# Kernel tuning notes

Hardware: AMD Instinct MI355X
Metric: run time of the kernel (lower is better)

Reference implementation:

```python
import jax, jax.numpy as jnp
import numpy as np

U, I, D, B, T = 100000, 50000, 64, 8192, 30
EUI, EII, L = 1600000, 800000, 2
LN_EPS = 1e-5
BEH_SCALE = 0.35
REG_COEF = 1e-4


def _ln(x, g, b):
    mu = jnp.mean(x, axis=-1, keepdims=True)
    var = jnp.mean((x - mu) ** 2, axis=-1, keepdims=True)
    return (x - mu) * jax.lax.rsqrt(var + LN_EPS) * g + b


def setup_inputs() -> dict:
    key = jax.random.key(0)
    ks = jax.random.split(key, 32)
    s = 0.1
    n = lambda k, shp: jax.random.normal(k, shp, dtype=jnp.float32) * s
    return {
        "user_emb": n(ks[0], (U, D)),
        "item_emb": n(ks[1], (I, D)),
        "beh_emb": n(ks[2], (4, D)),
        "t_w1": n(ks[3], (1, D)),
        "t_b1": jnp.zeros((D,), jnp.float32),
        "t_w2": n(ks[4], (D, D)),
        "t_b2": jnp.zeros((D,), jnp.float32),
        "gru_w_ih": n(ks[5], (D, 3 * D)),
        "gru_w_hh": n(ks[6], (D, 3 * D)),
        "gru_b_ih": jnp.zeros((3 * D,), jnp.float32),
        "gru_b_hh": jnp.zeros((3 * D,), jnp.float32),
        "gnn_user_w": n(ks[7], (L, D, D)),
        "gnn_user_b": jnp.zeros((L, D), jnp.float32),
        "gnn_item_w": n(ks[8], (L, D, D)),
        "gnn_item_b": jnp.zeros((L, D), jnp.float32),
        "ln_g": jnp.ones((D,), jnp.float32),
        "ln_b": jnp.zeros((D,), jnp.float32),
        "ui_vals": jax.random.uniform(ks[9], (EUI,), dtype=jnp.float32) * 0.1,
        "adj_vals": jax.random.uniform(ks[10], (EII,), dtype=jnp.float32) * 0.1,
        "seq_delta_days": jax.random.uniform(ks[11], (B, T), dtype=jnp.float32) * 100.0,
        "ui_rows": jax.random.randint(ks[12], (EUI,), 0, U),
        "ui_cols": jax.random.randint(ks[13], (EUI,), 0, I),
        "adj_rows": jax.random.randint(ks[14], (EII,), 0, I),
        "adj_cols": jax.random.randint(ks[15], (EII,), 0, I),
        "seq_items": jax.random.randint(ks[16], (B, T), 0, I),
        "seq_behaviors": jax.random.randint(ks[17], (B, T), 0, 4),
        "seq_len": jax.random.randint(ks[18], (B,), 1, T + 1),
        "user_idx": jax.random.randint(ks[19], (B,), 0, U),
        "pos_item_idx": jax.random.randint(ks[20], (B,), 0, I),
        "neg_item_idx": jax.random.randint(ks[21], (B,), 0, I),
        "pos_behavior": jax.random.randint(ks[22], (B,), 0, 4),
    }


def _forward(user_emb, item_emb, beh_emb, t_w1, t_b1, t_w2, t_b2,
             gru_w_ih, gru_w_hh, gru_b_ih, gru_b_hh,
             gnn_user_w, gnn_user_b, gnn_item_w, gnn_item_b,
             ln_g, ln_b, ui_vals, adj_vals, seq_delta_days,
             ui_rows, ui_cols, adj_rows, adj_cols,
             seq_items, seq_behaviors, seq_len,
             user_idx, pos_item_idx, neg_item_idx, pos_behavior):
    seg = jax.ops.segment_sum
    u, it = user_emb, item_emb
    # spatial propagation (sparse mm via edge-list segment sums); dropout off (eval)
    for l in range(L):
        agg_u = seg(ui_vals[:, None] * it[ui_cols], ui_rows, num_segments=U)       # ui_norm @ i
        agg_i_t = seg(adj_vals[:, None] * it[adj_cols], adj_rows, num_segments=I)  # item_adj @ i
        agg_i_u = seg(ui_vals[:, None] * u[ui_rows], ui_cols, num_segments=I)      # ui_norm.T @ u
        u = jax.nn.relu((u + agg_u) @ gnn_user_w[l] + gnn_user_b[l])
        it = jax.nn.relu((it + agg_i_t + agg_i_u) @ gnn_item_w[l] + gnn_item_b[l])
    # sequence encoding
    seq_x = it[seq_items] + BEH_SCALE * beh_emb[seq_behaviors]                     # [B,T,D]
    t_in = jnp.log1p(seq_delta_days)[..., None]                                    # [B,T,1]
    seq_x = seq_x + jax.nn.relu(t_in @ t_w1 + t_b1) @ t_w2 + t_b2
    seq_x = _ln(seq_x, ln_g, ln_b)
    mask = jnp.arange(T)[:, None] < seq_len[None, :]                               # [T,B]
    xs = jnp.transpose(seq_x, (1, 0, 2))                                           # [T,B,D]
    h0 = jnp.zeros((B, D), seq_x.dtype)

    def step(h, inputs):
        x_t, m_t = inputs
        gi = x_t @ gru_w_ih + gru_b_ih
        gh = h @ gru_w_hh + gru_b_hh
        i_r, i_z, i_n = jnp.split(gi, 3, axis=-1)
        h_r, h_z, h_n = jnp.split(gh, 3, axis=-1)
        r = jax.nn.sigmoid(i_r + h_r)
        z = jax.nn.sigmoid(i_z + h_z)
        nn_ = jnp.tanh(i_n + r * h_n)
        h_new = (1.0 - z) * nn_ + z * h
        return jnp.where(m_t[:, None], h_new, h), None

    seq_repr, _ = jax.lax.scan(step, h0, (xs, mask))                               # hidden at last valid step
    # BPR scoring
    u_final = _ln(u[user_idx] + seq_repr, ln_g, ln_b)
    pos = it[pos_item_idx]
    neg = it[neg_item_idx]
    pos_s = jnp.sum(u_final * pos, axis=-1)
    neg_s = jnp.sum(u_final * neg, axis=-1)
    w_map = jnp.array([1.0, 1.25, 1.6, 2.1], dtype=pos_s.dtype)
    bw = w_map[jnp.clip(pos_behavior, 0, 3)]
    bpr = jnp.mean(-jax.nn.log_sigmoid(pos_s - neg_s) * bw)
    reg = (jnp.mean(jnp.linalg.norm(u_final, axis=-1))
           + jnp.mean(jnp.linalg.norm(pos, axis=-1))
           + jnp.mean(jnp.linalg.norm(neg, axis=-1))) * REG_COEF
    return bpr + reg


def reference(user_emb, item_emb, beh_emb, t_w1, t_b1, t_w2, t_b2,
              gru_w_ih, gru_w_hh, gru_b_ih, gru_b_hh,
              gnn_user_w, gnn_user_b, gnn_item_w, gnn_item_b,
              ln_g, ln_b, ui_vals, adj_vals, seq_delta_days,
              ui_rows, ui_cols, adj_rows, adj_cols,
              seq_items, seq_behaviors, seq_len,
              user_idx, pos_item_idx, neg_item_idx, pos_behavior):
    return _forward(user_emb, item_emb, beh_emb, t_w1, t_b1, t_w2, t_b2,
                    gru_w_ih, gru_w_hh, gru_b_ih, gru_b_hh,
                    gnn_user_w, gnn_user_b, gnn_item_w, gnn_item_b,
                    ln_g, ln_b, ui_vals, adj_vals, seq_delta_days,
                    ui_rows, ui_cols, adj_rows, adj_cols,
                    seq_items, seq_behaviors, seq_len,
                    user_idx, pos_item_idx, neg_item_idx, pos_behavior)
```

## Files before the change

### kernel.cpp

```cpp
#include <hip/hip_runtime.h>
#include <math.h>

#define U_N 100000
#define I_N 50000
#define DD  64
#define BB  8192
#define TT  30
#define N_EUI 1600000
#define N_EII 800000
#define LN_EPS_ 1e-5f
#define BEH_SCALE_ 0.35f
#define REG_COEF_ 1e-4f

typedef unsigned short us_t;

__device__ __forceinline__ float wave_sum64(float v) {
#pragma unroll
  for (int o = 32; o > 0; o >>= 1) v += __shfl_xor(v, o, 64);
  return v;
}

__device__ __forceinline__ float rdlane(float v, int k) {
  return __int_as_float(__builtin_amdgcn_readlane(__float_as_int(v), k));
}

__device__ __forceinline__ us_t f2bf(float f) {
  unsigned u = __float_as_uint(f);
  u += 0x7fffu + ((u >> 16) & 1u);
  return (us_t)(u >> 16);
}
__device__ __forceinline__ float bf2f(us_t h) {
  return __uint_as_float((unsigned)h << 16);
}

__device__ __forceinline__ void fma4(float* acc, float s, float4 w4) {
  acc[0] = fmaf(s, w4.x, acc[0]);
  acc[1] = fmaf(s, w4.y, acc[1]);
  acc[2] = fmaf(s, w4.z, acc[2]);
  acc[3] = fmaf(s, w4.w, acc[3]);
}

__global__ __launch_bounds__(256) void to_bf16(const float* __restrict__ in,
                                               us_t* __restrict__ out,
                                               long n4) {
  for (long i = (long)blockIdx.x * blockDim.x + threadIdx.x; i < n4;
       i += (long)gridDim.x * blockDim.x) {
    float4 f = ((const float4*)in)[i];
    ushort4 o;
    o.x = f2bf(f.x); o.y = f2bf(f.y); o.z = f2bf(f.z); o.w = f2bf(f.w);
    ((ushort4*)out)[i] = o;
  }
}


__global__ __launch_bounds__(256) void hist_kernel(
    const int* __restrict__ rows, int nE, int* __restrict__ cnt) {
  for (long e = (long)blockIdx.x * blockDim.x + threadIdx.x; e < nE;
       e += (long)gridDim.x * blockDim.x)
    atomicAdd(&cnt[rows[e]], 1);
}

__global__ __launch_bounds__(1024) void ex_scan(
    const int* __restrict__ cnt, int n, int* __restrict__ offs,
    int* __restrict__ cursor) {
  __shared__ int part[1024];
  const int tid = threadIdx.x;
  const int chunk = (n + 1023) / 1024;
  const int lo = tid * chunk;
  const int hi = min(lo + chunk, n);
  int s = 0;
  for (int i = lo; i < hi; ++i) s += cnt[i];
  part[tid] = s;
  __syncthreads();
  for (int off = 1; off < 1024; off <<= 1) {
    int v = part[tid];
    int add = (tid >= off) ? part[tid - off] : 0;
    __syncthreads();
    part[tid] = v + add;
    __syncthreads();
  }
  int base = (tid == 0) ? 0 : part[tid - 1];
  for (int i = lo; i < hi; ++i) {
    int c = cnt[i];
    offs[i] = base;
    cursor[i] = base;
    base += c;
  }
  if (tid == 0) offs[n] = part[1023];
}

__global__ __launch_bounds__(256) void csr_fill(
    const int* __restrict__ drows, const int* __restrict__ srows,
    const float* __restrict__ vals, int nE, int* __restrict__ cursor,
    int2* __restrict__ pairs) {
  for (long e = (long)blockIdx.x * blockDim.x + threadIdx.x; e < nE;
       e += (long)gridDim.x * blockDim.x) {
    int d = drows[e];
    int pos = atomicAdd(&cursor[d], 1);
    pairs[pos] = make_int2(srows[e], __float_as_int(vals[e]));
  }
}


__global__ __launch_bounds__(256) void gnn_user_layer(
    const float* __restrict__ cur_u, const us_t* __restrict__ src_bf,
    const int* __restrict__ offs, const int2* __restrict__ pairs,
    const float* __restrict__ W, const float* __restrict__ bias,
    float* __restrict__ out, us_t* __restrict__ out_bf) {
  __shared__ float Wl[DD * DD];
  for (int i = threadIdx.x; i < DD * DD; i += blockDim.x) Wl[i] = W[i];
  __syncthreads();
  const int lane = threadIdx.x & 63;
  const float bn = bias[lane];
  long wid = ((long)blockIdx.x * blockDim.x + threadIdx.x) >> 6;
  long nw = ((long)gridDim.x * blockDim.x) >> 6;
  for (long r = wid; r < U_N; r += nw) {
    float acc = cur_u[r * DD + lane], acc2 = 0.f;
    int j = offs[r], j1 = offs[r + 1];
    for (; j + 1 < j1; j += 2) {
      int2 p0 = pairs[j], p1 = pairs[j + 1];
      acc = fmaf(__int_as_float(p0.y), bf2f(src_bf[(long)p0.x * DD + lane]), acc);
      acc2 = fmaf(__int_as_float(p1.y), bf2f(src_bf[(long)p1.x * DD + lane]), acc2);
    }
    if (j < j1) {
      int2 p = pairs[j];
      acc = fmaf(__int_as_float(p.y), bf2f(src_bf[(long)p.x * DD + lane]), acc);
    }
    acc += acc2;
    float y = bn;
#pragma unroll
    for (int k = 0; k < DD; ++k)
      y = fmaf(rdlane(acc, k), Wl[k * DD + lane], y);
    y = fmaxf(y, 0.f);
    out[r * DD + lane] = y;
    if (out_bf) out_bf[r * DD + lane] = f2bf(y);
  }
}

__global__ __launch_bounds__(256) void gnn_item_layer(
    const float* __restrict__ cur_it, const us_t* __restrict__ it_bf,
    const us_t* __restrict__ u_bf, const int* __restrict__ offsA,
    const int2* __restrict__ pairsA, const int* __restrict__ offsB,
    const int2* __restrict__ pairsB, const float* __restrict__ W,
    const float* __restrict__ bias, float* __restrict__ out,
    us_t* __restrict__ out_bf) {
  __shared__ float Wl[DD * DD];
  for (int i = threadIdx.x; i < DD * DD; i += blockDim.x) Wl[i] = W[i];
  __syncthreads();
  const int lane = threadIdx.x & 63;
  const float bn = bias[lane];
  long wid = ((long)blockIdx.x * blockDim.x + threadIdx.x) >> 6;
  long nw = ((long)gridDim.x * blockDim.x) >> 6;
  for (long r = wid; r < I_N; r += nw) {
    float acc = cur_it[r * DD + lane], acc2 = 0.f;
    int j = offsA[r], j1 = offsA[r + 1];
    for (; j + 1 < j1; j += 2) {
      int2 p0 = pairsA[j], p1 = pairsA[j + 1];
      acc = fmaf(__int_as_float(p0.y), bf2f(it_bf[(long)p0.x * DD + lane]), acc);
      acc2 = fmaf(__int_as_float(p1.y), bf2f(it_bf[(long)p1.x * DD + lane]), acc2);
    }
    if (j < j1) {
      int2 p = pairsA[j];
      acc = fmaf(__int_as_float(p.y), bf2f(it_bf[(long)p.x * DD + lane]), acc);
    }
    j = offsB[r];
    j1 = offsB[r + 1];
    for (; j + 1 < j1; j += 2) {
      int2 p0 = pairsB[j], p1 = pairsB[j + 1];
      acc = fmaf(__int_as_float(p0.y), bf2f(u_bf[(long)p0.x * DD + lane]), acc);
      acc2 = fmaf(__int_as_float(p1.y), bf2f(u_bf[(long)p1.x * DD + lane]), acc2);
    }
    if (j < j1) {
      int2 p = pairsB[j];
      acc = fmaf(__int_as_float(p.y), bf2f(u_bf[(long)p.x * DD + lane]), acc);
    }
    acc += acc2;
    float y = bn;
#pragma unroll
    for (int k = 0; k < DD; ++k)
      y = fmaf(rdlane(acc, k), Wl[k * DD + lane], y);
    y = fmaxf(y, 0.f);
    out[r * DD + lane] = y;
    if (out_bf) out_bf[r * DD + lane] = f2bf(y);
  }
}

__global__ __launch_bounds__(256) void gnn_user_sel(
    const float* __restrict__ u_a, const us_t* __restrict__ ita_bf,
    const int* __restrict__ user_idx, const int* __restrict__ offs,
    const int2* __restrict__ pairs, const float* __restrict__ W,
    const float* __restrict__ bias, float* __restrict__ out) {
  __shared__ float Wl[DD * DD];
  for (int i = threadIdx.x; i < DD * DD; i += blockDim.x) Wl[i] = W[i];
  __syncthreads();
  const int lane = threadIdx.x & 63;
  const float bn = bias[lane];
  long wid = ((long)blockIdx.x * blockDim.x + threadIdx.x) >> 6;
  long nw = ((long)gridDim.x * blockDim.x) >> 6;
  for (long b = wid; b < BB; b += nw) {
    int r = user_idx[b];
    float acc = u_a[(long)r * DD + lane], acc2 = 0.f;
    int j = offs[r], j1 = offs[r + 1];
    for (; j + 1 < j1; j += 2) {
      int2 p0 = pairs[j], p1 = pairs[j + 1];
      acc = fmaf(__int_as_float(p0.y), bf2f(ita_bf[(long)p0.x * DD + lane]), acc);
      acc2 = fmaf(__int_as_float(p1.y), bf2f(ita_bf[(long)p1.x * DD + lane]), acc2);
    }
    if (j < j1) {
      int2 p = pairs[j];
      acc = fmaf(__int_as_float(p.y), bf2f(ita_bf[(long)p.x * DD + lane]), acc);
    }
    acc += acc2;
    float y = bn;
#pragma unroll
    for (int k = 0; k < DD; ++k)
      y = fmaf(rdlane(acc, k), Wl[k * DD + lane], y);
    out[b * DD + lane] = fmaxf(y, 0.f);
  }
}


__global__ __launch_bounds__(256) void seq_encode_gi4(
    const float* __restrict__ itf, const float* __restrict__ beh_emb,
    const float* __restrict__ t_w1, const float* __restrict__ t_b1,
    const float* __restrict__ t_w2, const float* __restrict__ t_b2,
    const float* __restrict__ ln_g, const float* __restrict__ ln_b,
    const float* __restrict__ Wih, const float* __restrict__ bih,
    const float* __restrict__ delta, const int* __restrict__ items,
    const int* __restrict__ behs, us_t* __restrict__ gi) {
  __shared__ float W2q[DD * DD];
  __shared__ float WIq[192 * DD];
  for (int i = threadIdx.x; i < DD * DD; i += 256) {
    int k = i >> 6, c = i & 63;
    W2q[(k >> 2) * 256 + c * 4 + (k & 3)] = t_w2[i];
  }
  for (int i = threadIdx.x; i < DD * 192; i += 256) {
    int k = i / 192, c = i - k * 192;
    WIq[(k >> 2) * 768 + c * 4 + (k & 3)] = Wih[i];
  }
  __syncthreads();
  const int lane = threadIdx.x & 63;
  const float w1 = t_w1[lane], b1 = t_b1[lane], b2 = t_b2[lane];
  const float g = ln_g[lane], bo = ln_b[lane];
  const float bi0 = bih[lane], bi1 = bih[64 + lane], bi2 = bih[128 + lane];
  long wid = ((long)blockIdx.x * blockDim.x + threadIdx.x) >> 6;
  long nw = ((long)gridDim.x * blockDim.x) >> 6;
  const long NR = (long)BB * TT;
  for (long r4 = wid * 4; r4 < NR; r4 += nw * 4) {
    float xv[4], tmp[4];
#pragma unroll
    for (int i = 0; i < 4; ++i) {
      long r = r4 + i;
      int it = items[r];
      int bh = behs[r];
      xv[i] = itf[(long)it * DD + lane] + BEH_SCALE_ * beh_emb[bh * DD + lane];
      float tv = log1pf(delta[r]);
      tmp[i] = fmaxf(fmaf(tv, w1, b1), 0.f);
    }
    float y[4] = {b2, b2, b2, b2};
#pragma unroll 4
    for (int k4 = 0; k4 < 16; ++k4) {
      float4 w4 = *(const float4*)&W2q[k4 * 256 + lane * 4];
#pragma unroll
      for (int i = 0; i < 4; ++i) {
        y[i] = fmaf(rdlane(tmp[i], 4 * k4 + 0), w4.x, y[i]);
        y[i] = fmaf(rdlane(tmp[i], 4 * k4 + 1), w4.y, y[i]);
        y[i] = fmaf(rdlane(tmp[i], 4 * k4 + 2), w4.z, y[i]);
        y[i] = fmaf(rdlane(tmp[i], 4 * k4 + 3), w4.w, y[i]);
      }
    }
    float xo[4];
#pragma unroll
    for (int i = 0; i < 4; ++i) {
      float x = xv[i] + y[i];
      float mu = wave_sum64(x) * (1.f / DD);
      float xc = x - mu;
      float var = wave_sum64(xc * xc) * (1.f / DD);
      xo[i] = xc * rsqrtf(var + LN_EPS_) * g + bo;
    }
    float gA[4] = {bi0, bi0, bi0, bi0};
    float gB[4] = {bi1, bi1, bi1, bi1};
    float gC[4] = {bi2, bi2, bi2, bi2};
#pragma unroll 4
    for (int k4 = 0; k4 < 16; ++k4) {
      float4 wA = *(const float4*)&WIq[k4 * 768 + lane * 4];
      float4 wB = *(const float4*)&WIq[k4 * 768 + (64 + lane) * 4];
      float4 wC = *(const float4*)&WIq[k4 * 768 + (128 + lane) * 4];
#pragma unroll
      for (int i = 0; i < 4; ++i) {
        float s0 = rdlane(xo[i], 4 * k4 + 0);
        float s1 = rdlane(xo[i], 4 * k4 + 1);
        float s2 = rdlane(xo[i], 4 * k4 + 2);
        float s3 = rdlane(xo[i], 4 * k4 + 3);
        gA[i] = fmaf(s0, wA.x, gA[i]); gA[i] = fmaf(s1, wA.y, gA[i]);
        gA[i] = fmaf(s2, wA.z, gA[i]); gA[i] = fmaf(s3, wA.w, gA[i]);
        gB[i] = fmaf(s0, wB.x, gB[i]); gB[i] = fmaf(s1, wB.y, gB[i]);
        gB[i] = fmaf(s2, wB.z, gB[i]); gB[i] = fmaf(s3, wB.w, gB[i]);
        gC[i] = fmaf(s0, wC.x, gC[i]); gC[i] = fmaf(s1, wC.y, gC[i]);
        gC[i] = fmaf(s2, wC.z, gC[i]); gC[i] = fmaf(s3, wC.w, gC[i]);
      }
    }
#pragma unroll
    for (int i = 0; i < 4; ++i) {
      us_t* go = gi + (r4 + i) * 192;
      go[lane] = f2bf(gA[i]);
      go[64 + lane] = f2bf(gB[i]);
      go[128 + lane] = f2bf(gC[i]);
    }
  }
}

#define GHSTR 34

__global__ __launch_bounds__(256, 4) void gru_scan4(
    const us_t* __restrict__ gi, const float* __restrict__ Whh,
    const float* __restrict__ bhh, const int* __restrict__ seq_len,
    float* __restrict__ hfin) {
  __shared__ float sW[DD * 192];
  __shared__ float hT[DD * GHSTR];
  const int tid = threadIdx.x;
  for (int i = tid; i < DD * 192; i += 256) sW[i] = Whh[i];
  const int ct = tid & 15, rt = tid >> 4;
  const int d0 = ct * 4, r0 = rt * 2;
  const int row0 = blockIdx.x * 32;
  float bR[4], bZ[4], bN[4];
#pragma unroll
  for (int dd = 0; dd < 4; ++dd) {
    bR[dd] = bhh[d0 + dd];
    bZ[dd] = bhh[64 + d0 + dd];
    bN[dd] = bhh[128 + d0 + dd];
  }
  const int sl0 = seq_len[row0 + r0], sl1 = seq_len[row0 + r0 + 1];
  float h0[4] = {0.f, 0.f, 0.f, 0.f}, h1[4] = {0.f, 0.f, 0.f, 0.f};
  const us_t* ga = gi + (long)(row0 + r0) * TT * 192;
  const us_t* gb = gi + (long)(row0 + r0 + 1) * TT * 192;
  ushort4 pa0 = *(const ushort4*)(ga + d0);
  ushort4 pa1 = *(const ushort4*)(ga + 64 + d0);
  ushort4 pa2 = *(const ushort4*)(ga + 128 + d0);
  ushort4 pb0 = *(const ushort4*)(gb + d0);
  ushort4 pb1 = *(const ushort4*)(gb + 64 + d0);
  ushort4 pb2 = *(const ushort4*)(gb + 128 + d0);
  __syncthreads();

  for (int t = 0; t < TT; ++t) {
#pragma unroll
    for (int dd = 0; dd < 4; ++dd) {
      hT[(d0 + dd) * GHSTR + r0] = h0[dd];
      hT[(d0 + dd) * GHSTR + r0 + 1] = h1[dd];
    }
    ushort4 na0, na1, na2, nb0, nb1, nb2;
    if (t + 1 < TT) {
      const us_t* a = ga + (long)(t + 1) * 192;
      const us_t* b = gb + (long)(t + 1) * 192;
      na0 = *(const ushort4*)(a + d0);
      na1 = *(const ushort4*)(a + 64 + d0);
      na2 = *(const ushort4*)(a + 128 + d0);
      nb0 = *(const ushort4*)(b + d0);
      nb1 = *(const ushort4*)(b + 64 + d0);
      nb2 = *(const ushort4*)(b + 128 + d0);
    }
    float aR0[4], aZ0[4], aN0[4], aH0[4];
    float aR1[4], aZ1[4], aN1[4], aH1[4];
    aR0[0] = bR[0] + bf2f(pa0.x); aR0[1] = bR[1] + bf2f(pa0.y);
    aR0[2] = bR[2] + bf2f(pa0.z); aR0[3] = bR[3] + bf2f(pa0.w);
    aZ0[0] = bZ[0] + bf2f(pa1.x); aZ0[1] = bZ[1] + bf2f(pa1.y);
    aZ0[2] = bZ[2] + bf2f(pa1.z); aZ0[3] = bZ[3] + bf2f(pa1.w);
    aN0[0] = bf2f(pa2.x); aN0[1] = bf2f(pa2.y);
    aN0[2] = bf2f(pa2.z); aN0[3] = bf2f(pa2.w);
    aR1[0] = bR[0] + bf2f(pb0.x); aR1[1] = bR[1] + bf2f(pb0.y);
    aR1[2] = bR[2] + bf2f(pb0.z); aR1[3] = bR[3] + bf2f(pb0.w);
    aZ1[0] = bZ[0] + bf2f(pb1.x); aZ1[1] = bZ[1] + bf2f(pb1.y);
    aZ1[2] = bZ[2] + bf2f(pb1.z); aZ1[3] = bZ[3] + bf2f(pb1.w);
    aN1[0] = bf2f(pb2.x); aN1[1] = bf2f(pb2.y);
    aN1[2] = bf2f(pb2.z); aN1[3] = bf2f(pb2.w);
#pragma unroll
    for (int dd = 0; dd < 4; ++dd) {
      aH0[dd] = bN[dd];
      aH1[dd] = bN[dd];
    }
    __syncthreads();
#pragma unroll 8
    for (int k = 0; k < DD; ++k) {
      float2 hh = *(const float2*)&hT[k * GHSTR + r0];
      float4 wr4 = *(const float4*)&sW[k * 192 + d0];
      float4 wz4 = *(const float4*)&sW[k * 192 + 64 + d0];
      float4 wn4 = *(const float4*)&sW[k * 192 + 128 + d0];
      fma4(aR0, hh.x, wr4);
      fma4(aR1, hh.y, wr4);
      fma4(aZ0, hh.x, wz4);
      fma4(aZ1, hh.y, wz4);
      fma4(aH0, hh.x, wn4);
      fma4(aH1, hh.y, wn4);
    }
    const bool m0 = t < sl0, m1 = t < sl1;
#pragma unroll
    for (int dd = 0; dd < 4; ++dd) {
      float rg = 1.f / (1.f + __expf(-aR0[dd]));
      float zg = 1.f / (1.f + __expf(-aZ0[dd]));
      float ng = tanhf(fmaf(rg, aH0[dd], aN0[dd]));
      float hn = fmaf(zg, h0[dd] - ng, ng);
      h0[dd] = m0 ? hn : h0[dd];
      rg = 1.f / (1.f + __expf(-aR1[dd]));
      zg = 1.f / (1.f + __expf(-aZ1[dd]));
      ng = tanhf(fmaf(rg, aH1[dd], aN1[dd]));
      hn = fmaf(zg, h1[dd] - ng, ng);
      h1[dd] = m1 ? hn : h1[dd];
    }
    pa0 = na0; pa1 = na1; pa2 = na2;
    pb0 = nb0; pb1 = nb1; pb2 = nb2;
    __syncthreads();
  }
#pragma unroll
  for (int dd = 0; dd < 4; ++dd) {
    hfin[(long)(row0 + r0) * DD + d0 + dd] = h0[dd];
    hfin[(long)(row0 + r0 + 1) * DD + d0 + dd] = h1[dd];
  }
}


__global__ __launch_bounds__(256) void final_score(
    const float* __restrict__ u_sel, const float* __restrict__ itf,
    const float* __restrict__ hfin, const float* __restrict__ ln_g,
    const float* __restrict__ ln_b, const int* __restrict__ pos_idx,
    const int* __restrict__ neg_idx, const int* __restrict__ pos_beh,
    float* __restrict__ out) {
  __shared__ float partial[4];
  const int lane = threadIdx.x & 63;
  const int wv = threadIdx.x >> 6;
  const float g = ln_g[lane], bo = ln_b[lane];
  float local = 0.f;
  int wid = blockIdx.x * 4 + wv;
  int nw = gridDim.x * 4;
  for (int r = wid; r < BB; r += nw) {
    float uf = u_sel[(long)r * DD + lane] + hfin[(long)r * DD + lane];
    float mu = wave_sum64(uf) * (1.f / DD);
    float xc = uf - mu;
    float var = wave_sum64(xc * xc) * (1.f / DD);
    float un = xc * rsqrtf(var + LN_EPS_) * g + bo;
    float pv = itf[(long)pos_idx[r] * DD + lane];
    float nv = itf[(long)neg_idx[r] * DD + lane];
    float ps = wave_sum64(un * pv);
    float ns = wave_sum64(un * nv);
    float n1 = wave_sum64(un * un);
    float n2 = wave_sum64(pv * pv);
    float n3 = wave_sum64(nv * nv);
    float d = ps - ns;
    float sp = fmaxf(-d, 0.f) + log1pf(__expf(-fabsf(d)));
    int pb = pos_beh[r];
    pb = pb < 0 ? 0 : (pb > 3 ? 3 : pb);
    float bw = pb == 0 ? 1.0f : (pb == 1 ? 1.25f : (pb == 2 ? 1.6f : 2.1f));
    local += sp * bw + REG_COEF_ * (sqrtf(n1) + sqrtf(n2) + sqrtf(n3));
  }
  if (lane == 0) partial[wv] = local;
  __syncthreads();
  if (threadIdx.x == 0) {
    float s = partial[0] + partial[1] + partial[2] + partial[3];
    atomicAdd(out, s * (1.f / BB));
  }
}

extern "C" void kernel_launch(void* const* d_in, const int* in_sizes, int n_in,
                              void* d_out, int out_size, void* d_ws,
                              size_t ws_size, hipStream_t stream) {
  const float* user_emb = (const float*)d_in[0];
  const float* item_emb = (const float*)d_in[1];
  const float* beh_emb = (const float*)d_in[2];
  const float* t_w1 = (const float*)d_in[3];
  const float* t_b1 = (const float*)d_in[4];
  const float* t_w2 = (const float*)d_in[5];
  const float* t_b2 = (const float*)d_in[6];
  const float* gru_w_ih = (const float*)d_in[7];
  const float* gru_w_hh = (const float*)d_in[8];
  const float* gru_b_ih = (const float*)d_in[9];
  const float* gru_b_hh = (const float*)d_in[10];
  const float* gnn_user_w = (const float*)d_in[11];
  const float* gnn_user_b = (const float*)d_in[12];
  const float* gnn_item_w = (const float*)d_in[13];
  const float* gnn_item_b = (const float*)d_in[14];
  const float* ln_g = (const float*)d_in[15];
  const float* ln_b = (const float*)d_in[16];
  const float* ui_vals = (const float*)d_in[17];
  const float* adj_vals = (const float*)d_in[18];
  const float* seq_delta = (const float*)d_in[19];
  const int* ui_rows = (const int*)d_in[20];
  const int* ui_cols = (const int*)d_in[21];
  const int* adj_rows = (const int*)d_in[22];
  const int* adj_cols = (const int*)d_in[23];
  const int* seq_items = (const int*)d_in[24];
  const int* seq_behaviors = (const int*)d_in[25];
  const int* seq_len = (const int*)d_in[26];
  const int* user_idx = (const int*)d_in[27];
  const int* pos_item_idx = (const int*)d_in[28];
  const int* neg_item_idx = (const int*)d_in[29];
  const int* pos_behavior = (const int*)d_in[30];

  float* ws = (float*)d_ws;
  float* u_a = ws;
  float* it_a = u_a + (long)U_N * DD;
  float* it_b = it_a + (long)I_N * DD;
  float* hfin = it_b + (long)I_N * DD;
  float* u_sel = hfin + (long)BB * DD;
  float* end_f = u_sel + (long)BB * DD;

  int2* pairs_ui_row = (int2*)end_f;
  int2* pairs_ui_col = pairs_ui_row + N_EUI;
  int2* pairs_adj = pairs_ui_col + N_EUI;

  us_t* gi = (us_t*)(pairs_adj + N_EII);
  us_t* user_bf = gi + (long)BB * TT * 192;
  us_t* item_bf = user_bf + (long)U_N * DD;
  us_t* ua_bf = item_bf + (long)I_N * DD;
  us_t* ita_bf = ua_bf + (long)U_N * DD;

  int* offs_ui_row = (int*)(ita_bf + (long)I_N * DD);
  int* offs_ui_col = offs_ui_row + (U_N + 1);
  int* offs_adj = offs_ui_col + (I_N + 1);
  int* cur_ui_row = offs_adj + (I_N + 1);
  int* cur_ui_col = cur_ui_row + U_N;
  int* cur_adj = cur_ui_col + I_N;

  hipMemsetAsync(d_out, 0, (size_t)out_size * sizeof(float), stream);
  hipMemsetAsync(cur_ui_row, 0, (size_t)(U_N + I_N + I_N) * sizeof(int),
                 stream);

  to_bf16<<<1024, 256, 0, stream>>>(user_emb, user_bf, (long)U_N * DD / 4);
  to_bf16<<<1024, 256, 0, stream>>>(item_emb, item_bf, (long)I_N * DD / 4);

  hist_kernel<<<2048, 256, 0, stream>>>(ui_rows, N_EUI, cur_ui_row);
  hist_kernel<<<2048, 256, 0, stream>>>(ui_cols, N_EUI, cur_ui_col);
  hist_kernel<<<1024, 256, 0, stream>>>(adj_rows, N_EII, cur_adj);
  ex_scan<<<1, 1024, 0, stream>>>(cur_ui_row, U_N, offs_ui_row, cur_ui_row);
  ex_scan<<<1, 1024, 0, stream>>>(cur_ui_col, I_N, offs_ui_col, cur_ui_col);
  ex_scan<<<1, 1024, 0, stream>>>(cur_adj, I_N, offs_adj, cur_adj);
  csr_fill<<<2048, 256, 0, stream>>>(ui_rows, ui_cols, ui_vals, N_EUI,
                                     cur_ui_row, pairs_ui_row);
  csr_fill<<<2048, 256, 0, stream>>>(ui_cols, ui_rows, ui_vals, N_EUI,
                                     cur_ui_col, pairs_ui_col);
  csr_fill<<<1024, 256, 0, stream>>>(adj_rows, adj_cols, adj_vals, N_EII,
                                     cur_adj, pairs_adj);

  gnn_user_layer<<<2048, 256, 0, stream>>>(user_emb, item_bf, offs_ui_row,
                                           pairs_ui_row, gnn_user_w,
                                           gnn_user_b, u_a, ua_bf);
  gnn_item_layer<<<2048, 256, 0, stream>>>(item_emb, item_bf, user_bf,
                                           offs_adj, pairs_adj, offs_ui_col,
                                           pairs_ui_col, gnn_item_w,
                                           gnn_item_b, it_a, ita_bf);
  gnn_item_layer<<<2048, 256, 0, stream>>>(it_a, ita_bf, ua_bf, offs_adj,
                                           pairs_adj, offs_ui_col,
                                           pairs_ui_col, gnn_item_w + DD * DD,
                                           gnn_item_b + DD, it_b, nullptr);
  gnn_user_sel<<<512, 256, 0, stream>>>(u_a, ita_bf, user_idx, offs_ui_row,
                                        pairs_ui_row, gnn_user_w + DD * DD,
                                        gnn_user_b + DD, u_sel);

  seq_encode_gi4<<<512, 256, 0, stream>>>(it_b, beh_emb, t_w1, t_b1, t_w2,
                                          t_b2, ln_g, ln_b, gru_w_ih,
                                          gru_b_ih, seq_delta, seq_items,
                                          seq_behaviors, gi);

  gru_scan4<<<BB / 32, 256, 0, stream>>>(gi, gru_w_hh, gru_b_hh, seq_len,
                                         hfin);

  final_score<<<256, 256, 0, stream>>>(u_sel, it_b, hfin, ln_g, ln_b,
                                       pos_item_idx, neg_item_idx,
                                       pos_behavior, (float*)d_out);
}
```

Measured before the change: 2.167 ms.

## Use bf16 MFMA for sequence encoder matmuls and merge CSR build kernels

Rewrites the sequence encoder so the time-MLP projection and the GRU input projection run as 16x16x32 bf16 MFMA tiles over 16-row groups. Activations are staged through a swizzled LDS buffer and weights are preconverted to bf16 fragments. Separately, the three histogram, scan and fill launches for CSR construction are each merged into one launch to cut launch overhead. This adds bf16 rounding on the inputs to the time-MLP matmul and more block-level syncs per tile, and the grid is fixed at 480 blocks to cover all rows exactly.

```diff
diff --git a/kernel.cpp b/kernel.cpp
--- a/kernel.cpp
+++ b/kernel.cpp
@@ -13,6 +13,8 @@
 #define REG_COEF_ 1e-4f
 
 typedef unsigned short us_t;
+typedef __attribute__((ext_vector_type(8))) short bf16x8;
+typedef __attribute__((ext_vector_type(4))) float f32x4;
 
 __device__ __forceinline__ float wave_sum64(float v) {
 #pragma unroll
@@ -53,17 +55,22 @@
 }
 
 
-__global__ __launch_bounds__(256) void hist_kernel(
-    const int* __restrict__ rows, int nE, int* __restrict__ cnt) {
-  for (long e = (long)blockIdx.x * blockDim.x + threadIdx.x; e < nE;
-       e += (long)gridDim.x * blockDim.x)
+__global__ __launch_bounds__(256) void hist3(
+    const int* __restrict__ r0, const int* __restrict__ r1,
+    const int* __restrict__ r2, int* __restrict__ c0, int* __restrict__ c1,
+    int* __restrict__ c2) {
+  int b = blockIdx.x;
+  const int* rows; int* cnt; int n, base, nb;
+  if (b < 1024) { rows = r0; cnt = c0; n = N_EUI; base = 0; nb = 1024; }
+  else if (b < 2048) { rows = r1; cnt = c1; n = N_EUI; base = 1024; nb = 1024; }
+  else { rows = r2; cnt = c2; n = N_EII; base = 2048; nb = 512; }
+  for (long e = (long)(b - base) * 256 + threadIdx.x; e < n;
+       e += (long)nb * 256)
     atomicAdd(&cnt[rows[e]], 1);
 }
 
-__global__ __launch_bounds__(1024) void ex_scan(
-    const int* __restrict__ cnt, int n, int* __restrict__ offs,
-    int* __restrict__ cursor) {
-  __shared__ int part[1024];
+__device__ __forceinline__ void ex_scan_body(const int* cnt, int n, int* offs,
+                                             int* cursor, int* part) {
   const int tid = threadIdx.x;
   const int chunk = (n + 1023) / 1024;
   const int lo = tid * chunk;
@@ -89,12 +96,34 @@
   if (tid == 0) offs[n] = part[1023];
 }
 
-__global__ __launch_bounds__(256) void csr_fill(
-    const int* __restrict__ drows, const int* __restrict__ srows,
-    const float* __restrict__ vals, int nE, int* __restrict__ cursor,
-    int2* __restrict__ pairs) {
-  for (long e = (long)blockIdx.x * blockDim.x + threadIdx.x; e < nE;
-       e += (long)gridDim.x * blockDim.x) {
+__global__ __launch_bounds__(1024) void scan3(
+    int* __restrict__ c0, int* __restrict__ o0, int* __restrict__ c1,
+    int* __restrict__ o1, int* __restrict__ c2, int* __restrict__ o2) {
+  __shared__ int part[1024];
+  if (blockIdx.x == 0) ex_scan_body(c0, U_N, o0, c0, part);
+  else if (blockIdx.x == 1) ex_scan_body(c1, I_N, o1, c1, part);
+  else ex_scan_body(c2, I_N, o2, c2, part);
+}
+
+__global__ __launch_bounds__(256) void fill3(
+    const int* __restrict__ d0, const int* __restrict__ s0,
+    const float* __restrict__ v0, int* __restrict__ cu0,
+    int2* __restrict__ p0, const int* __restrict__ d1,
+    const int* __restrict__ s1, const float* __restrict__ v1,
+    int* __restrict__ cu1, int2* __restrict__ p1, const int* __restrict__ d2,
+    const int* __restrict__ s2, const float* __restrict__ v2,
+    int* __restrict__ cu2, int2* __restrict__ p2) {
+  int b = blockIdx.x;
+  const int *drows, *srows; const float* vals; int* cursor; int2* pairs;
+  int n, base, nb;
+  if (b < 1024) { drows = d0; srows = s0; vals = v0; cursor = cu0; pairs = p0;
+                  n = N_EUI; base = 0; nb = 1024; }
+  else if (b < 2048) { drows = d1; srows = s1; vals = v1; cursor = cu1;
+                       pairs = p1; n = N_EUI; base = 1024; nb = 1024; }
+  else { drows = d2; srows = s2; vals = v2; cursor = cu2; pairs = p2;
+         n = N_EII; base = 2048; nb = 512; }
+  for (long e = (long)(b - base) * 256 + threadIdx.x; e < n;
+       e += (long)nb * 256) {
     int d = drows[e];
     int pos = atomicAdd(&cursor[d], 1);
     pairs[pos] = make_int2(srows[e], __float_as_int(vals[e]));
@@ -220,7 +249,7 @@
 }
 
 
-__global__ __launch_bounds__(256) void seq_encode_gi4(
+__global__ __launch_bounds__(256) void seq_mfma(
     const float* __restrict__ itf, const float* __restrict__ beh_emb,
     const float* __restrict__ t_w1, const float* __restrict__ t_b1,
     const float* __restrict__ t_w2, const float* __restrict__ t_b2,
@@ -228,85 +257,107 @@
     const float* __restrict__ Wih, const float* __restrict__ bih,
     const float* __restrict__ delta, const int* __restrict__ items,
     const int* __restrict__ behs, us_t* __restrict__ gi) {
-  __shared__ float W2q[DD * DD];
-  __shared__ float WIq[192 * DD];
-  for (int i = threadIdx.x; i < DD * DD; i += 256) {
-    int k = i >> 6, c = i & 63;
-    W2q[(k >> 2) * 256 + c * 4 + (k & 3)] = t_w2[i];
-  }
-  for (int i = threadIdx.x; i < DD * 192; i += 256) {
-    int k = i / 192, c = i - k * 192;
-    WIq[(k >> 2) * 768 + c * 4 + (k & 3)] = Wih[i];
+  __shared__ __attribute__((aligned(16))) us_t WB2s[8 * 512];
+  __shared__ __attribute__((aligned(16))) us_t WBIs[24 * 512];
+  __shared__ __attribute__((aligned(16))) us_t AFs[4][1024];
+  __shared__ __attribute__((aligned(16))) float yTs[4][16 * 68];
+  const int tid = threadIdx.x;
+  for (int idx = tid; idx < 8 * 512; idx += 256) {
+    int f = idx >> 9, l = (idx >> 3) & 63, j = idx & 7;
+    int ct = f >> 1, kt = f & 1;
+    int k = kt * 32 + ((l >> 4) << 3) + j;
+    int c = (ct << 4) + (l & 15);
+    WB2s[idx] = f2bf(t_w2[k * 64 + c]);
+  }
+  for (int idx = tid; idx < 24 * 512; idx += 256) {
+    int f = idx >> 9, l = (idx >> 3) & 63, j = idx & 7;
+    int ct = f >> 1, kt = f & 1;
+    int k = kt * 32 + ((l >> 4) << 3) + j;
+    int c = (ct << 4) + (l & 15);
+    WBIs[idx] = f2bf(Wih[k * 192 + c]);
   }
   __syncthreads();
-  const int lane = threadIdx.x & 63;
-  const float w1 = t_w1[lane], b1 = t_b1[lane], b2 = t_b2[lane];
-  const float g = ln_g[lane], bo = ln_b[lane];
-  const float bi0 = bih[lane], bi1 = bih[64 + lane], bi2 = bih[128 + lane];
-  long wid = ((long)blockIdx.x * blockDim.x + threadIdx.x) >> 6;
-  long nw = ((long)gridDim.x * blockDim.x) >> 6;
-  const long NR = (long)BB * TT;
-  for (long r4 = wid * 4; r4 < NR; r4 += nw * 4) {
-    float xv[4], tmp[4];
-#pragma unroll
-    for (int i = 0; i < 4; ++i) {
-      long r = r4 + i;
-      int it = items[r];
-      int bh = behs[r];
-      xv[i] = itf[(long)it * DD + lane] + BEH_SCALE_ * beh_emb[bh * DD + lane];
-      float tv = log1pf(delta[r]);
-      tmp[i] = fmaxf(fmaf(tv, w1, b1), 0.f);
-    }
-    float y[4] = {b2, b2, b2, b2};
-#pragma unroll 4
-    for (int k4 = 0; k4 < 16; ++k4) {
-      float4 w4 = *(const float4*)&W2q[k4 * 256 + lane * 4];
-#pragma unroll
-      for (int i = 0; i < 4; ++i) {
-        y[i] = fmaf(rdlane(tmp[i], 4 * k4 + 0), w4.x, y[i]);
-        y[i] = fmaf(rdlane(tmp[i], 4 * k4 + 1), w4.y, y[i]);
-        y[i] = fmaf(rdlane(tmp[i], 4 * k4 + 2), w4.z, y[i]);
-        y[i] = fmaf(rdlane(tmp[i], 4 * k4 + 3), w4.w, y[i]);
+
+  const int lane = tid & 63;
+  const int wv = tid >> 6;
+  const float w1l = t_w1[lane], b1l = t_b1[lane], b2l = t_b2[lane];
+  const float gl = ln_g[lane], bol = ln_b[lane];
+  const int colL = lane & 15;
+  const int rbase = (lane >> 4) * 4;
+  float biv[12];
+#pragma unroll
+  for (int ct = 0; ct < 12; ++ct) biv[ct] = bih[ct * 16 + colL];
+
+  us_t* AF = AFs[wv];
+  float* yT = yTs[wv];
+  const long wgl = (long)blockIdx.x * 4 + wv;
+
+  const int row = lane & 15;
+  const int a_off0 = ((row * 8 + 0 + (lane >> 4)) ^ (row & 7)) * 8;
+  const int a_off1 = ((row * 8 + 4 + (lane >> 4)) ^ (row & 7)) * 8;
+
+  for (int it8 = 0; it8 < 8; ++it8) {
+    const long tile = wgl * 8 + it8;
+    const long r0 = tile * 16;
+    float xbr[16];
+#pragma unroll
+    for (int r = 0; r < 16; ++r) {
+      long ridx = r0 + r;
+      int itm = items[ridx];
+      int bh = behs[ridx];
+      xbr[r] = itf[(long)itm * DD + lane] +
+               BEH_SCALE_ * beh_emb[bh * DD + lane];
+      float tv = log1pf(delta[ridx]);
+      float tmp = fmaxf(fmaf(tv, w1l, b1l), 0.f);
+      int u = (r * 8 + (lane >> 3)) ^ (r & 7);
+      AF[u * 8 + (lane & 7)] = f2bf(tmp);
+    }
+    __syncthreads();
+    {
+      bf16x8 aA = *(const bf16x8*)&AF[a_off0];
+      bf16x8 aB = *(const bf16x8*)&AF[a_off1];
+#pragma unroll
+      for (int ct = 0; ct < 4; ++ct) {
+        f32x4 acc = {0.f, 0.f, 0.f, 0.f};
+        bf16x8 b0 = *(const bf16x8*)&WB2s[(ct * 2 + 0) * 512 + lane * 8];
+        bf16x8 b1 = *(const bf16x8*)&WB2s[(ct * 2 + 1) * 512 + lane * 8];
+        acc = __builtin_amdgcn_mfma_f32_16x16x32_bf16(aA, b0, acc, 0, 0, 0);
+        acc = __builtin_amdgcn_mfma_f32_16x16x32_bf16(aB, b1, acc, 0, 0, 0);
+        int col = ct * 16 + colL;
+#pragma unroll
+        for (int i = 0; i < 4; ++i) yT[(rbase + i) * 68 + col] = acc[i];
       }
     }
-    float xo[4];
-#pragma unroll
-    for (int i = 0; i < 4; ++i) {
-      float x = xv[i] + y[i];
+    __syncthreads();
+#pragma unroll
+    for (int r = 0; r < 16; ++r) {
+      float x = xbr[r] + yT[r * 68 + lane] + b2l;
       float mu = wave_sum64(x) * (1.f / DD);
       float xc = x - mu;
       float var = wave_sum64(xc * xc) * (1.f / DD);
-      xo[i] = xc * rsqrtf(var + LN_EPS_) * g + bo;
-    }
-    float gA[4] = {bi0, bi0, bi0, bi0};
-    float gB[4] = {bi1, bi1, bi1, bi1};
-    float gC[4] = {bi2, bi2, bi2, bi2};
-#pragma unroll 4
-    for (int k4 = 0; k4 < 16; ++k4) {
-      float4 wA = *(const float4*)&WIq[k4 * 768 + lane * 4];
-      float4 wB = *(const float4*)&WIq[k4 * 768 + (64 + lane) * 4];
-      float4 wC = *(const float4*)&WIq[k4 * 768 + (128 + lane) * 4];
-#pragma unroll
-      for (int i = 0; i < 4; ++i) {
-        float s0 = rdlane(xo[i], 4 * k4 + 0);
-        float s1 = rdlane(xo[i], 4 * k4 + 1);
-        float s2 = rdlane(xo[i], 4 * k4 + 2);
-        float s3 = rdlane(xo[i], 4 * k4 + 3);
-        gA[i] = fmaf(s0, wA.x, gA[i]); gA[i] = fmaf(s1, wA.y, gA[i]);
-        gA[i] = fmaf(s2, wA.z, gA[i]); gA[i] = fmaf(s3, wA.w, gA[i]);
-        gB[i] = fmaf(s0, wB.x, gB[i]); gB[i] = fmaf(s1, wB.y, gB[i]);
-        gB[i] = fmaf(s2, wB.z, gB[i]); gB[i] = fmaf(s3, wB.w, gB[i]);
-        gC[i] = fmaf(s0, wC.x, gC[i]); gC[i] = fmaf(s1, wC.y, gC[i]);
-        gC[i] = fmaf(s2, wC.z, gC[i]); gC[i] = fmaf(s3, wC.w, gC[i]);
+      float xo = xc * rsqrtf(var + LN_EPS_) * gl + bol;
+      int u = (r * 8 + (lane >> 3)) ^ (r & 7);
+      AF[u * 8 + (lane & 7)] = f2bf(xo);
+    }
+    __syncthreads();
+    {
+      bf16x8 aA = *(const bf16x8*)&AF[a_off0];
+      bf16x8 aB = *(const bf16x8*)&AF[a_off1];
+      us_t* go = gi + r0 * 192;
+#pragma unroll
+      for (int ct = 0; ct < 12; ++ct) {
+        float bv = biv[ct];
+        f32x4 acc = {bv, bv, bv, bv};
+        bf16x8 b0 = *(const bf16x8*)&WBIs[(ct * 2 + 0) * 512 + lane * 8];
+        bf16x8 b1 = *(const bf16x8*)&WBIs[(ct * 2 + 1) * 512 + lane * 8];
+        acc = __builtin_amdgcn_mfma_f32_16x16x32_bf16(aA, b0, acc, 0, 0, 0);
+        acc = __builtin_amdgcn_mfma_f32_16x16x32_bf16(aB, b1, acc, 0, 0, 0);
+#pragma unroll
+        for (int i = 0; i < 4; ++i)
+          go[(long)(rbase + i) * 192 + ct * 16 + colL] = f2bf(acc[i]);
       }
     }
-#pragma unroll
-    for (int i = 0; i < 4; ++i) {
-      us_t* go = gi + (r4 + i) * 192;
-      go[lane] = f2bf(gA[i]);
-      go[64 + lane] = f2bf(gB[i]);
-      go[128 + lane] = f2bf(gC[i]);
-    }
+    __syncthreads();
   }
 }
 
@@ -526,18 +577,14 @@
   to_bf16<<<1024, 256, 0, stream>>>(user_emb, user_bf, (long)U_N * DD / 4);
   to_bf16<<<1024, 256, 0, stream>>>(item_emb, item_bf, (long)I_N * DD / 4);
 
-  hist_kernel<<<2048, 256, 0, stream>>>(ui_rows, N_EUI, cur_ui_row);
-  hist_kernel<<<2048, 256, 0, stream>>>(ui_cols, N_EUI, cur_ui_col);
-  hist_kernel<<<1024, 256, 0, stream>>>(adj_rows, N_EII, cur_adj);
-  ex_scan<<<1, 1024, 0, stream>>>(cur_ui_row, U_N, offs_ui_row, cur_ui_row);
-  ex_scan<<<1, 1024, 0, stream>>>(cur_ui_col, I_N, offs_ui_col, cur_ui_col);
-  ex_scan<<<1, 1024, 0, stream>>>(cur_adj, I_N, offs_adj, cur_adj);
-  csr_fill<<<2048, 256, 0, stream>>>(ui_rows, ui_cols, ui_vals, N_EUI,
-                                     cur_ui_row, pairs_ui_row);
-  csr_fill<<<2048, 256, 0, stream>>>(ui_cols, ui_rows, ui_vals, N_EUI,
-                                     cur_ui_col, pairs_ui_col);
-  csr_fill<<<1024, 256, 0, stream>>>(adj_rows, adj_cols, adj_vals, N_EII,
-                                     cur_adj, pairs_adj);
+  hist3<<<2560, 256, 0, stream>>>(ui_rows, ui_cols, adj_rows, cur_ui_row,
+                                  cur_ui_col, cur_adj);
+  scan3<<<3, 1024, 0, stream>>>(cur_ui_row, offs_ui_row, cur_ui_col,
+                                offs_ui_col, cur_adj, offs_adj);
+  fill3<<<2560, 256, 0, stream>>>(ui_rows, ui_cols, ui_vals, cur_ui_row,
+                                  pairs_ui_row, ui_cols, ui_rows, ui_vals,
+                                  cur_ui_col, pairs_ui_col, adj_rows, adj_cols,
+                                  adj_vals, cur_adj, pairs_adj);
 
   gnn_user_layer<<<2048, 256, 0, stream>>>(user_emb, item_bf, offs_ui_row,
                                            pairs_ui_row, gnn_user_w,
@@ -554,10 +601,9 @@
                                         pairs_ui_row, gnn_user_w + DD * DD,
                                         gnn_user_b + DD, u_sel);
 
-  seq_encode_gi4<<<512, 256, 0, stream>>>(it_b, beh_emb, t_w1, t_b1, t_w2,
-                                          t_b2, ln_g, ln_b, gru_w_ih,
-                                          gru_b_ih, seq_delta, seq_items,
-                                          seq_behaviors, gi);
+  seq_mfma<<<480, 256, 0, stream>>>(it_b, beh_emb, t_w1, t_b1, t_w2, t_b2,
+                                    ln_g, ln_b, gru_w_ih, gru_b_ih, seq_delta,
+                                    seq_items, seq_behaviors, gi);
 
   gru_scan4<<<BB / 32, 256, 0, stream>>>(gi, gru_w_hh, gru_b_hh, seq_len,
                                          hfin);
```

After: 1.804 ms. 1.2x faster.
